# Kernel tuning notes

Hardware: AMD Instinct MI355X
Metric: run time of the kernel (lower is better)

Reference implementation:

```python
import jax, jax.numpy as jnp
import numpy as np


def setup_inputs() -> dict:
    key = jax.random.key(0)
    ks = jax.random.split(key, 12)
    M, B, N, FD, BD, BVD, H = 4096, 8, 512, 128, 128, 6, 64
    return {
        "f_pre_in": jax.random.normal(ks[0], (M, FD), jnp.float32),
        "f_pre_batch": jnp.sort(jax.random.randint(ks[1], (M,), 0, B)),
        "b_pre_in": jax.random.normal(ks[2], (B, BD, N), jnp.float32),
        "bv_in": jax.random.normal(ks[3], (B, BVD, N), jnp.float32),
        "Wf": jax.random.normal(ks[4], (H, FD), jnp.float32) * 0.05,
        "bf": jax.random.normal(ks[5], (H,), jnp.float32) * 0.05,
        "Wb": jax.random.normal(ks[6], (H, BD), jnp.float32) * 0.05,
        "bb": jax.random.normal(ks[7], (H,), jnp.float32) * 0.05,
        "Wbv": jax.random.normal(ks[8], (H, BVD), jnp.float32) * 0.05,
        "bbv": jax.random.normal(ks[9], (H,), jnp.float32) * 0.05,
        "Wo": jax.random.normal(ks[10], (H, 2 * H), jnp.float32) * 0.05,
        "bo": jax.random.normal(ks[11], (H,), jnp.float32) * 0.05,
    }


def reference(f_pre_in, f_pre_batch, b_pre_in, bv_in, Wf, bf, Wb, bb, Wbv, bbv, Wo, bo):
    # 1x1 Conv1d == channel matmul.
    H = Wf.shape[0]
    h2 = H // 2
    scale = jnp.sqrt(jnp.asarray(H, jnp.float32))  # sqrt(hidden_size)
    f = Wf @ f_pre_in.T + bf[:, None]                                  # (H, M)
    b_feat = jnp.einsum('hd,bdn->bhn', Wb, b_pre_in) + bb[None, :, None]   # (B, H, N)
    bv_feat = jnp.einsum('hc,bcn->bhn', Wbv, bv_in) + bbv[None, :, None]   # (B, H, N)
    # Per-node gather of that node's graph boundary features (f_pre_batch is sorted,
    # so per-node order == torch's per-batch concat order).
    be = b_feat[f_pre_batch, :h2]    # (M, h2, N)
    bg = b_feat[f_pre_batch, h2:]    # (M, h2, N)
    bvg = bv_feat[f_pre_batch]       # (M, H, N)
    # Cross-attention: softmax over the N boundary positions (torch dim=0 of (N, n_b)).
    w_euc = jax.nn.softmax(jnp.einsum('mhn,hm->mn', be, f[:h2]) / scale, axis=-1)  # (M, N)
    w_geo = jax.nn.softmax(jnp.einsum('mhn,hm->mn', bg, f[h2:]) / scale, axis=-1)  # (M, N)
    out_euc = jnp.einsum('mhn,mn->mh', bvg, w_euc)   # (M, H)
    out_geo = jnp.einsum('mhn,mn->mh', bvg, w_geo)   # (M, H)
    cat = jnp.concatenate([out_euc, out_geo], axis=1)  # (M, 2H)
    return cat @ Wo.T + bo                              # (M, H)
```

## Files before the change

kernel.cpp:

```cpp
#include <hip/hip_runtime.h>

#define M_TOT 4096
#define B_TOT 8
#define N_TOT 512
#define FD    128
#define BD    128
#define BVD   6
#define H     64
#define H2    32
#define MAX_TILES 264

__device__ __forceinline__ int lb_dev(const int* __restrict__ arr, int n, int v) {
    int lo = 0, hi = n;
    while (lo < hi) { int mid = (lo + hi) >> 1; if (arr[mid] < v) lo = mid + 1; else hi = mid; }
    return lo;
}

__global__ __launch_bounds__(256) void k_pre(const float* __restrict__ f_pre_in,
                                             const int*   __restrict__ batch,
                                             const float* __restrict__ b_pre_in,
                                             const float* __restrict__ bv_in,
                                             const float* __restrict__ Wf,
                                             const float* __restrict__ bf,
                                             const float* __restrict__ Wb,
                                             const float* __restrict__ bb,
                                             const float* __restrict__ Wbv,
                                             const float* __restrict__ bbv,
                                             float* __restrict__ f_mh,
                                             float* __restrict__ b_feat,
                                             float* __restrict__ bv_T,
                                             int4*  __restrict__ table) {
    __shared__ float fpre[16 * 132];
    __shared__ float WfT[128 * 68];
    __shared__ float ws2[2 * 132];
    const int t = threadIdx.x;
    const int blk = blockIdx.x;

    if (blk < 256) {
        const int m0 = blk * 16;
        for (int i = t; i < 16 * FD; i += 256)
            fpre[(i >> 7) * 132 + (i & 127)] = f_pre_in[(size_t)m0 * FD + i];
        for (int i = t; i < H * FD; i += 256)
            WfT[(i & 127) * 68 + (i >> 7)] = Wf[i];
        __syncthreads();
        const int mi = t >> 4;
        const int h4 = (t & 15) * 4;
        float a0 = bf[h4], a1 = bf[h4 + 1], a2 = bf[h4 + 2], a3 = bf[h4 + 3];
#pragma unroll 4
        for (int d4 = 0; d4 < 32; ++d4) {
            const float4 fp = *(const float4*)&fpre[mi * 132 + d4 * 4];
            const float* fpp = &fp.x;
#pragma unroll
            for (int i = 0; i < 4; ++i) {
                const float4 wv = *(const float4*)&WfT[(d4 * 4 + i) * 68 + h4];
                const float f = fpp[i];
                a0 += f * wv.x; a1 += f * wv.y; a2 += f * wv.z; a3 += f * wv.w;
            }
        }
        *(float4*)&f_mh[(size_t)(m0 + mi) * H + h4] = make_float4(a0, a1, a2, a3);
    } else if (blk < 512) {
        const int idx = blk - 256;
        const int b  = idx >> 5;
        const int h0 = (idx & 31) * 2;
        ws2[(t >> 7) * 132 + (t & 127)] = Wb[(h0 + (t >> 7)) * BD + (t & 127)];
        __syncthreads();
        const int hi = t >> 7;
        const int n4 = (t & 127) * 4;
        const float bias = bb[h0 + hi];
        float a0 = bias, a1 = bias, a2 = bias, a3 = bias;
        const float* src = b_pre_in + (size_t)b * BD * N_TOT + n4;
        const float* wp = &ws2[hi * 132];
#pragma unroll 8
        for (int d = 0; d < BD; ++d) {
            const float wv = wp[d];
            const float4 v = *(const float4*)(src + (size_t)d * N_TOT);
            a0 += wv * v.x; a1 += wv * v.y; a2 += wv * v.z; a3 += wv * v.w;
        }
        *(float4*)&b_feat[((size_t)b * H + h0 + hi) * N_TOT + n4] = make_float4(a0, a1, a2, a3);
    } else if (blk < 768) {
        const int idx = blk - 512;
        const int b  = idx >> 5;
        const int n0 = (idx & 31) * 16;
        const int h  = t & 63;
        const int nq = t >> 6;
        float wreg[BVD];
#pragma unroll
        for (int c = 0; c < BVD; ++c) wreg[c] = Wbv[h * BVD + c];
        const float bias = bbv[h];
        const float* src = bv_in + (size_t)b * BVD * N_TOT;
#pragma unroll
        for (int j = 0; j < 4; ++j) {
            const int n = n0 + nq * 4 + j;
            float acc = bias;
#pragma unroll
            for (int c = 0; c < BVD; ++c) acc += wreg[c] * src[c * N_TOT + n];
            bv_T[((size_t)b * N_TOT + n) * H + h] = acc;
        }
    } else {
        int starts[9];
#pragma unroll
        for (int b = 0; b <= 8; ++b) starts[b] = lb_dev(batch, M_TOT, b);
        int pre[9]; pre[0] = 0;
#pragma unroll
        for (int b = 0; b < 8; ++b) pre[b + 1] = pre[b] + (starts[b + 1] - starts[b] + 15) / 16;
        const int total = pre[8];
        for (int idx = t; idx < MAX_TILES; idx += 256) {
            int4 e = make_int4(0, 0, 0, 0);
            if (idx < total) {
                int b = 0;
                while (pre[b + 1] <= idx) ++b;
                const int r0 = starts[b] + (idx - pre[b]) * 16;
                e.x = b; e.y = r0; e.z = min(16, starts[b + 1] - r0);
            }
            table[idx] = e;
        }
    }
}

__device__ __forceinline__ float wave_sum64(float x) {
#pragma unroll
    for (int m = 1; m < 64; m <<= 1) x += __shfl_xor(x, m);
    return x;
}

__global__ __launch_bounds__(512, 4) void k_main(const float* __restrict__ f_mh,
                                                 const float* __restrict__ b_feat,
                                                 const float* __restrict__ bv_T,
                                                 const int4*  __restrict__ table,
                                                 float* __restrict__ pOut,
                                                 float* __restrict__ pSum) {
    __shared__ float fT[64 * 20];
    __shared__ float bFbv[64 * 133];
    __shared__ float wE[16 * 132];
    __shared__ float wG[16 * 132];
    __shared__ float rowsum[16][2];

    const int t = threadIdx.x;
    const int q    = blockIdx.x & 3;
    const int tile = blockIdx.x >> 2;
    const int4 te = table[tile];
    const int b = te.x, m0 = te.y, nr = te.z;
    if (nr == 0) return;
    const int nb = q * 128;

    for (int i = t; i < 16 * H; i += 512) {
        const int r = i >> 6, h = i & 63;
        fT[h * 20 + r] = f_mh[(size_t)(m0 + min(r, nr - 1)) * H + h];
    }
    {
        const float* src = b_feat + (size_t)b * H * N_TOT + nb;
        for (int i = t; i < 2048; i += 512) {
            const int h = i >> 5, n4 = (i & 31) * 4;
            *(float4*)&bFbv[h * 132 + n4] = *(const float4*)&src[(size_t)h * N_TOT + n4];
        }
    }
    if (t < 32) rowsum[t >> 1][t & 1] = 0.f;
    __syncthreads();

    const int lane = t & 63;
    {
        const int n_l = t & 127;
        const int rgs = t >> 7;
        float se[4] = {0.f, 0.f, 0.f, 0.f}, sg[4] = {0.f, 0.f, 0.f, 0.f};
#pragma unroll 8
        for (int h = 0; h < H2; ++h) {
            const float bE = bFbv[h * 132 + n_l];
            const float bG = bFbv[(h + 32) * 132 + n_l];
            const float4 fe = *(const float4*)&fT[h * 20 + rgs * 4];
            const float4 fg = *(const float4*)&fT[(h + 32) * 20 + rgs * 4];
            se[0] += fe.x * bE; se[1] += fe.y * bE; se[2] += fe.z * bE; se[3] += fe.w * bE;
            sg[0] += fg.x * bG; sg[1] += fg.y * bG; sg[2] += fg.z * bG; sg[3] += fg.w * bG;
        }
        float we[4], wg[4];
#pragma unroll
        for (int j = 0; j < 4; ++j) {
            we[j] = __expf(se[j] * 0.125f);
            wg[j] = __expf(sg[j] * 0.125f);
        }
#pragma unroll
        for (int j = 0; j < 4; ++j) {
            const float sE = wave_sum64(we[j]);
            const float sG = wave_sum64(wg[j]);
            if (lane == 0) {
                atomicAdd(&rowsum[rgs * 4 + j][0], sE);
                atomicAdd(&rowsum[rgs * 4 + j][1], sG);
            }
            wE[(rgs * 4 + j) * 132 + n_l] = we[j];
            wG[(rgs * 4 + j) * 132 + n_l] = wg[j];
        }
    }
    __syncthreads();

    {
        const float* src = bv_T + ((size_t)b * N_TOT + nb) * H;
        for (int i = t; i < 2048; i += 512) {
            const int n_li = i >> 4, h4 = (i & 15) * 4;
            const float4 v = *(const float4*)&src[(size_t)n_li * H + h4];
            bFbv[(h4 + 0) * 133 + n_li] = v.x;
            bFbv[(h4 + 1) * 133 + n_li] = v.y;
            bFbv[(h4 + 2) * 133 + n_li] = v.z;
            bFbv[(h4 + 3) * 133 + n_li] = v.w;
        }
    }
    __syncthreads();

    if (t < 32) {
        const int r = t >> 1, eg = t & 1;
        if (r < nr) pSum[((size_t)q * M_TOT + m0 + r) * 2 + eg] = rowsum[r][eg];
    }

    {
        const int ns = t & 3, hg = (t >> 2) & 15, rgp = t >> 6;
        float aE[2][4] = {{0.f,0.f,0.f,0.f},{0.f,0.f,0.f,0.f}};
        float aG[2][4] = {{0.f,0.f,0.f,0.f},{0.f,0.f,0.f,0.f}};
#pragma unroll 4
        for (int i = 0; i < 32; ++i) {
            const int n = ns + 4 * i;
            const float we0 = wE[(rgp * 2 + 0) * 132 + n];
            const float we1 = wE[(rgp * 2 + 1) * 132 + n];
            const float wg0 = wG[(rgp * 2 + 0) * 132 + n];
            const float wg1 = wG[(rgp * 2 + 1) * 132 + n];
            float bv4[4];
#pragma unroll
            for (int c = 0; c < 4; ++c) bv4[c] = bFbv[(hg * 4 + c) * 133 + n];
#pragma unroll
            for (int c = 0; c < 4; ++c) {
                aE[0][c] += we0 * bv4[c];
                aE[1][c] += we1 * bv4[c];
                aG[0][c] += wg0 * bv4[c];
                aG[1][c] += wg1 * bv4[c];
            }
        }
#pragma unroll
        for (int j = 0; j < 2; ++j)
#pragma unroll
            for (int c = 0; c < 4; ++c) {
                aE[j][c] += __shfl_xor(aE[j][c], 1); aE[j][c] += __shfl_xor(aE[j][c], 2);
                aG[j][c] += __shfl_xor(aG[j][c], 1); aG[j][c] += __shfl_xor(aG[j][c], 2);
            }
        if (ns == 0) {
#pragma unroll
            for (int j = 0; j < 2; ++j) {
                const int r = rgp * 2 + j;
                if (r < nr) {
                    float* dst = pOut + ((size_t)q * M_TOT + m0 + r) * 128;
                    *(float4*)&dst[hg * 4]      = make_float4(aE[j][0], aE[j][1], aE[j][2], aE[j][3]);
                    *(float4*)&dst[64 + hg * 4] = make_float4(aG[j][0], aG[j][1], aG[j][2], aG[j][3]);
                }
            }
        }
    }
}

__global__ __launch_bounds__(256) void k_merge(const float* __restrict__ pOut,
                                               const float* __restrict__ pSum,
                                               const float* __restrict__ Wo,
                                               const float* __restrict__ bo,
                                               float* __restrict__ out) {
    __shared__ float WoT[128 * 68];
    __shared__ float cat[16 * 132];
    __shared__ float rinv[16][2];
    const int t = threadIdx.x;
    const int m0 = blockIdx.x * 16;

    for (int i = t; i < H * 2 * H; i += 256)
        WoT[(i & 127) * 68 + (i >> 7)] = Wo[i];
    if (t < 32) {
        const int r = t >> 1, eg = t & 1;
        float s = 0.f;
#pragma unroll
        for (int qq = 0; qq < 4; ++qq) s += pSum[((size_t)qq * M_TOT + m0 + r) * 2 + eg];
        rinv[r][eg] = 1.0f / s;
    }
    __syncthreads();

    for (int i = t; i < 512; i += 256) {
        const int r = i >> 5, k4 = (i & 31) * 4;
        float4 s = make_float4(0.f, 0.f, 0.f, 0.f);
#pragma unroll
        for (int qq = 0; qq < 4; ++qq) {
            const float4 v = *(const float4*)&pOut[(((size_t)qq * M_TOT + m0 + r) * 128) + k4];
            s.x += v.x; s.y += v.y; s.z += v.z; s.w += v.w;
        }
        const float inv = rinv[r][k4 >= 64];
        *(float4*)&cat[r * 132 + k4] = make_float4(s.x * inv, s.y * inv, s.z * inv, s.w * inv);
    }
    __syncthreads();

    const int mi = t >> 4;
    const int j4 = (t & 15) * 4;
    float a0 = bo[j4], a1 = bo[j4 + 1], a2 = bo[j4 + 2], a3 = bo[j4 + 3];
#pragma unroll 4
    for (int k4s = 0; k4s < 32; ++k4s) {
        const float4 c4 = *(const float4*)&cat[mi * 132 + 4 * k4s];
        const float* cp = &c4.x;
#pragma unroll
        for (int i = 0; i < 4; ++i) {
            const float4 wv = *(const float4*)&WoT[(4 * k4s + i) * 68 + j4];
            const float c = cp[i];
            a0 += c * wv.x; a1 += c * wv.y; a2 += c * wv.z; a3 += c * wv.w;
        }
    }
    *(float4*)&out[(size_t)(m0 + mi) * H + j4] = make_float4(a0, a1, a2, a3);
}

extern "C" void kernel_launch(void* const* d_in, const int* in_sizes, int n_in,
                              void* d_out, int out_size, void* d_ws, size_t ws_size,
                              hipStream_t stream) {
    const float* f_pre_in = (const float*)d_in[0];
    const int*   f_batch  = (const int*)  d_in[1];
    const float* b_pre_in = (const float*)d_in[2];
    const float* bv_in    = (const float*)d_in[3];
    const float* Wf       = (const float*)d_in[4];
    const float* bf       = (const float*)d_in[5];
    const float* Wb       = (const float*)d_in[6];
    const float* bb       = (const float*)d_in[7];
    const float* Wbv      = (const float*)d_in[8];
    const float* bbv      = (const float*)d_in[9];
    const float* Wo       = (const float*)d_in[10];
    const float* bo       = (const float*)d_in[11];
    float* out = (float*)d_out;

    float* f_mh   = (float*)d_ws;
    float* b_feat = f_mh + (size_t)M_TOT * H;
    float* bv_T   = b_feat + (size_t)B_TOT * H * N_TOT;
    float* pOut   = bv_T + (size_t)B_TOT * N_TOT * H;
    float* pSum   = pOut + (size_t)4 * M_TOT * 128;
    int4*  table  = (int4*)(pSum + (size_t)4 * M_TOT * 2);

    k_pre  <<<769, 256, 0, stream>>>(f_pre_in, f_batch, b_pre_in, bv_in,
                                     Wf, bf, Wb, bb, Wbv, bbv,
                                     f_mh, b_feat, bv_T, table);
    k_main <<<4 * MAX_TILES, 512, 0, stream>>>(f_mh, b_feat, bv_T, table, pOut, pSum);
    k_merge<<<256, 256, 0, stream>>>(pOut, pSum, Wo, bo, out);
}
```

Baseline: 135.5 us.

## Rewrite attention core with bf16 MFMA and fuse merge/output projection into main kernel

```diff
diff --git a/kernel.cpp b/kernel.cpp
--- a/kernel.cpp
+++ b/kernel.cpp
@@ -7,8 +7,19 @@
 #define BD    128
 #define BVD   6
 #define H     64
-#define H2    32
 #define MAX_TILES 264
+
+typedef short short8 __attribute__((ext_vector_type(8)));
+typedef float floatx4 __attribute__((ext_vector_type(4)));
+
+__device__ __forceinline__ unsigned short f2bf(float x) {
+    union { float f; unsigned int u; } v; v.f = x;
+    return (unsigned short)((v.u + 0x7fffu + ((v.u >> 16) & 1u)) >> 16);
+}
+__device__ __forceinline__ float bf2f(unsigned short u) {
+    union { unsigned int u32; float f; } v; v.u32 = ((unsigned int)u) << 16;
+    return v.f;
+}
 
 __device__ __forceinline__ int lb_dev(const int* __restrict__ arr, int n, int v) {
     int lo = 0, hi = n;
@@ -26,17 +37,19 @@
                                              const float* __restrict__ bb,
                                              const float* __restrict__ Wbv,
                                              const float* __restrict__ bbv,
-                                             float* __restrict__ f_mh,
-                                             float* __restrict__ b_feat,
-                                             float* __restrict__ bv_T,
+                                             const float* __restrict__ Wo,
+                                             unsigned short* __restrict__ f_bf,
+                                             unsigned short* __restrict__ bFT_bf,
+                                             unsigned short* __restrict__ bv_bf,
+                                             unsigned short* __restrict__ Wo_bf,
                                              int4*  __restrict__ table) {
-    __shared__ float fpre[16 * 132];
-    __shared__ float WfT[128 * 68];
-    __shared__ float ws2[2 * 132];
+    __shared__ __align__(16) char sm[43264];
     const int t = threadIdx.x;
     const int blk = blockIdx.x;
 
     if (blk < 256) {
+        float* fpre = (float*)sm;
+        float* WfT  = (float*)(sm + 8448);
         const int m0 = blk * 16;
         for (int i = t; i < 16 * FD; i += 256)
             fpre[(i >> 7) * 132 + (i & 127)] = f_pre_in[(size_t)m0 * FD + i];
@@ -57,45 +70,54 @@
                 a0 += f * wv.x; a1 += f * wv.y; a2 += f * wv.z; a3 += f * wv.w;
             }
         }
-        *(float4*)&f_mh[(size_t)(m0 + mi) * H + h4] = make_float4(a0, a1, a2, a3);
+        ushort4 o; o.x = f2bf(a0); o.y = f2bf(a1); o.z = f2bf(a2); o.w = f2bf(a3);
+        *(ushort4*)&f_bf[(size_t)(m0 + mi) * H + h4] = o;
     } else if (blk < 512) {
+        float* Wb_l = (float*)sm;
+        float* bp   = (float*)(sm + 33024);
         const int idx = blk - 256;
         const int b  = idx >> 5;
-        const int h0 = (idx & 31) * 2;
-        ws2[(t >> 7) * 132 + (t & 127)] = Wb[(h0 + (t >> 7)) * BD + (t & 127)];
+        const int n0 = (idx & 31) * 16;
+        for (int i = t; i < H * BD; i += 256)
+            Wb_l[(i >> 7) * 129 + (i & 127)] = Wb[i];
+        for (int i = t; i < BD * 16; i += 256)
+            bp[(i >> 4) * 17 + (i & 15)] =
+                b_pre_in[(size_t)b * BD * N_TOT + (size_t)(i >> 4) * N_TOT + n0 + (i & 15)];
         __syncthreads();
-        const int hi = t >> 7;
-        const int n4 = (t & 127) * 4;
-        const float bias = bb[h0 + hi];
-        float a0 = bias, a1 = bias, a2 = bias, a3 = bias;
-        const float* src = b_pre_in + (size_t)b * BD * N_TOT + n4;
-        const float* wp = &ws2[hi * 132];
+        const int h  = t & 63;
+        const int nl = t >> 6;
+        const float bias = bb[h];
+        float acc[4] = {bias, bias, bias, bias};
+        const float* wr = &Wb_l[h * 129];
 #pragma unroll 8
         for (int d = 0; d < BD; ++d) {
-            const float wv = wp[d];
-            const float4 v = *(const float4*)(src + (size_t)d * N_TOT);
-            a0 += wv * v.x; a1 += wv * v.y; a2 += wv * v.z; a3 += wv * v.w;
-        }
-        *(float4*)&b_feat[((size_t)b * H + h0 + hi) * N_TOT + n4] = make_float4(a0, a1, a2, a3);
+            const float w = wr[d];
+            acc[0] += w * bp[d * 17 + nl];
+            acc[1] += w * bp[d * 17 + nl + 4];
+            acc[2] += w * bp[d * 17 + nl + 8];
+            acc[3] += w * bp[d * 17 + nl + 12];
+        }
+#pragma unroll
+        for (int j = 0; j < 4; ++j)
+            bFT_bf[((size_t)b * N_TOT + n0 + nl + 4 * j) * H + h] = f2bf(acc[j]);
     } else if (blk < 768) {
         const int idx = blk - 512;
         const int b  = idx >> 5;
-        const int n0 = (idx & 31) * 16;
-        const int h  = t & 63;
-        const int nq = t >> 6;
-        float wreg[BVD];
-#pragma unroll
-        for (int c = 0; c < BVD; ++c) wreg[c] = Wbv[h * BVD + c];
+        const int h  = (idx & 31) * 2 + (t >> 7);
+        const int n4 = (t & 127) * 4;
+        float w[BVD];
+#pragma unroll
+        for (int c = 0; c < BVD; ++c) w[c] = Wbv[h * BVD + c];
         const float bias = bbv[h];
-        const float* src = bv_in + (size_t)b * BVD * N_TOT;
-#pragma unroll
-        for (int j = 0; j < 4; ++j) {
-            const int n = n0 + nq * 4 + j;
-            float acc = bias;
-#pragma unroll
-            for (int c = 0; c < BVD; ++c) acc += wreg[c] * src[c * N_TOT + n];
-            bv_T[((size_t)b * N_TOT + n) * H + h] = acc;
-        }
+        float a0 = bias, a1 = bias, a2 = bias, a3 = bias;
+        const float* src = bv_in + (size_t)b * BVD * N_TOT + n4;
+#pragma unroll
+        for (int c = 0; c < BVD; ++c) {
+            const float4 v = *(const float4*)(src + c * N_TOT);
+            a0 += w[c] * v.x; a1 += w[c] * v.y; a2 += w[c] * v.z; a3 += w[c] * v.w;
+        }
+        ushort4 o; o.x = f2bf(a0); o.y = f2bf(a1); o.z = f2bf(a2); o.w = f2bf(a3);
+        *(ushort4*)&bv_bf[((size_t)b * H + h) * N_TOT + n4] = o;
     } else {
         int starts[9];
 #pragma unroll
@@ -114,194 +136,125 @@
             }
             table[idx] = e;
         }
-    }
-}
-
-__device__ __forceinline__ float wave_sum64(float x) {
-#pragma unroll
-    for (int m = 1; m < 64; m <<= 1) x += __shfl_xor(x, m);
-    return x;
-}
-
-__global__ __launch_bounds__(512, 4) void k_main(const float* __restrict__ f_mh,
-                                                 const float* __restrict__ b_feat,
-                                                 const float* __restrict__ bv_T,
-                                                 const int4*  __restrict__ table,
-                                                 float* __restrict__ pOut,
-                                                 float* __restrict__ pSum) {
-    __shared__ float fT[64 * 20];
-    __shared__ float bFbv[64 * 133];
-    __shared__ float wE[16 * 132];
-    __shared__ float wG[16 * 132];
-    __shared__ float rowsum[16][2];
+        for (int i = t; i < H * 2 * H; i += 256) Wo_bf[i] = f2bf(Wo[i]);
+    }
+}
+
+__global__ __launch_bounds__(256) void k_main(const unsigned short* __restrict__ f_bf,
+                                              const unsigned short* __restrict__ bFT_bf,
+                                              const unsigned short* __restrict__ bv_bf,
+                                              const unsigned short* __restrict__ Wo_bf,
+                                              const float* __restrict__ bo,
+                                              const int4*  __restrict__ table,
+                                              float* __restrict__ out) {
+    __shared__ __align__(16) char wreg[4][8704];
+    __shared__ __align__(16) float rowsumP[4][2][16];
+    __shared__ __align__(16) unsigned short cat_l[16 * 136];
 
     const int t = threadIdx.x;
-    const int q    = blockIdx.x & 3;
-    const int tile = blockIdx.x >> 2;
-    const int4 te = table[tile];
+    const int wave = t >> 6, l = t & 63, quad = l >> 4, s = l & 15;
+    const int4 te = table[blockIdx.x];
     const int b = te.x, m0 = te.y, nr = te.z;
     if (nr == 0) return;
-    const int nb = q * 128;
-
-    for (int i = t; i < 16 * H; i += 512) {
-        const int r = i >> 6, h = i & 63;
-        fT[h * 20 + r] = f_mh[(size_t)(m0 + min(r, nr - 1)) * H + h];
+
+    unsigned short* Wl = (unsigned short*)&wreg[wave][0];
+    const floatx4 zero = {0.f, 0.f, 0.f, 0.f};
+
+    const int rclamp = (s < nr) ? s : (nr - 1);
+    const unsigned short* fptr = f_bf + (size_t)(m0 + rclamp) * H + quad * 8;
+    const short8 fE = *(const short8*)(fptr);
+    const short8 fG = *(const short8*)(fptr + 32);
+
+    const unsigned short* bA = bFT_bf + ((size_t)b * N_TOT + wave * 128 + s) * H + quad * 8;
+    floatx4 dE[8], dG[8];
+#pragma unroll
+    for (int c = 0; c < 8; ++c) {
+        const short8 aE = *(const short8*)(bA + (size_t)c * 16 * H);
+        const short8 aG = *(const short8*)(bA + (size_t)c * 16 * H + 32);
+        dE[c] = __builtin_amdgcn_mfma_f32_16x16x32_bf16(aE, fE, zero, 0, 0, 0);
+        dG[c] = __builtin_amdgcn_mfma_f32_16x16x32_bf16(aG, fG, zero, 0, 0, 0);
+    }
+
+    float rsE = 0.f, rsG = 0.f;
+#pragma unroll
+    for (int c = 0; c < 8; ++c) {
+        ushort4 pE, pG;
+        unsigned short u;
+        u = f2bf(__expf(dE[c][0] * 0.125f)); rsE += bf2f(u); pE.x = u;
+        u = f2bf(__expf(dE[c][1] * 0.125f)); rsE += bf2f(u); pE.y = u;
+        u = f2bf(__expf(dE[c][2] * 0.125f)); rsE += bf2f(u); pE.z = u;
+        u = f2bf(__expf(dE[c][3] * 0.125f)); rsE += bf2f(u); pE.w = u;
+        u = f2bf(__expf(dG[c][0] * 0.125f)); rsG += bf2f(u); pG.x = u;
+        u = f2bf(__expf(dG[c][1] * 0.125f)); rsG += bf2f(u); pG.y = u;
+        u = f2bf(__expf(dG[c][2] * 0.125f)); rsG += bf2f(u); pG.z = u;
+        u = f2bf(__expf(dG[c][3] * 0.125f)); rsG += bf2f(u); pG.w = u;
+        *(ushort4*)&Wl[s * 136 + c * 16 + quad * 4]        = pE;
+        *(ushort4*)&Wl[2176 + s * 136 + c * 16 + quad * 4] = pG;
+    }
+    rsE += __shfl_xor(rsE, 16); rsE += __shfl_xor(rsE, 32);
+    rsG += __shfl_xor(rsG, 16); rsG += __shfl_xor(rsG, 32);
+    if (l < 16) { rowsumP[wave][0][s] = rsE; rowsumP[wave][1][s] = rsG; }
+
+    floatx4 oE[4] = {zero, zero, zero, zero};
+    floatx4 oG[4] = {zero, zero, zero, zero};
+#pragma unroll
+    for (int kc = 0; kc < 4; ++kc) {
+        const short8 aE = *(const short8*)&Wl[s * 136 + kc * 32 + quad * 8];
+        const short8 aG = *(const short8*)&Wl[2176 + s * 136 + kc * 32 + quad * 8];
+#pragma unroll
+        for (int hc = 0; hc < 4; ++hc) {
+            const short8 bvf = *(const short8*)(bv_bf +
+                ((size_t)b * H + hc * 16 + s) * N_TOT + wave * 128 + kc * 32 + quad * 8);
+            oE[hc] = __builtin_amdgcn_mfma_f32_16x16x32_bf16(aE, bvf, oE[hc], 0, 0, 0);
+            oG[hc] = __builtin_amdgcn_mfma_f32_16x16x32_bf16(aG, bvf, oG[hc], 0, 0, 0);
+        }
     }
     {
-        const float* src = b_feat + (size_t)b * H * N_TOT + nb;
-        for (int i = t; i < 2048; i += 512) {
-            const int h = i >> 5, n4 = (i & 31) * 4;
-            *(float4*)&bFbv[h * 132 + n4] = *(const float4*)&src[(size_t)h * N_TOT + n4];
-        }
-    }
-    if (t < 32) rowsum[t >> 1][t & 1] = 0.f;
+        float* Op = (float*)&wreg[wave][0];
+#pragma unroll
+        for (int hc = 0; hc < 4; ++hc) {
+            *(floatx4*)&Op[(hc * 16 + s) * 16 + quad * 4]        = oE[hc];
+            *(floatx4*)&Op[1024 + (hc * 16 + s) * 16 + quad * 4] = oG[hc];
+        }
+    }
     __syncthreads();
 
-    const int lane = t & 63;
     {
-        const int n_l = t & 127;
-        const int rgs = t >> 7;
-        float se[4] = {0.f, 0.f, 0.f, 0.f}, sg[4] = {0.f, 0.f, 0.f, 0.f};
-#pragma unroll 8
-        for (int h = 0; h < H2; ++h) {
-            const float bE = bFbv[h * 132 + n_l];
-            const float bG = bFbv[(h + 32) * 132 + n_l];
-            const float4 fe = *(const float4*)&fT[h * 20 + rgs * 4];
-            const float4 fg = *(const float4*)&fT[(h + 32) * 20 + rgs * 4];
-            se[0] += fe.x * bE; se[1] += fe.y * bE; se[2] += fe.z * bE; se[3] += fe.w * bE;
-            sg[0] += fg.x * bG; sg[1] += fg.y * bG; sg[2] += fg.z * bG; sg[3] += fg.w * bG;
-        }
-        float we[4], wg[4];
-#pragma unroll
-        for (int j = 0; j < 4; ++j) {
-            we[j] = __expf(se[j] * 0.125f);
-            wg[j] = __expf(sg[j] * 0.125f);
-        }
-#pragma unroll
-        for (int j = 0; j < 4; ++j) {
-            const float sE = wave_sum64(we[j]);
-            const float sG = wave_sum64(wg[j]);
-            if (lane == 0) {
-                atomicAdd(&rowsum[rgs * 4 + j][0], sE);
-                atomicAdd(&rowsum[rgs * 4 + j][1], sG);
-            }
-            wE[(rgs * 4 + j) * 132 + n_l] = we[j];
-            wG[(rgs * 4 + j) * 132 + n_l] = wg[j];
+        const int h  = t >> 2;
+        const int r4 = (t & 3) * 4;
+        floatx4 sE = zero, sG = zero, rE = zero, rG = zero;
+#pragma unroll
+        for (int w = 0; w < 4; ++w) {
+            const float* opw = (const float*)&wreg[w][0];
+            sE += *(const floatx4*)&opw[h * 16 + r4];
+            sG += *(const floatx4*)&opw[1024 + h * 16 + r4];
+            rE += *(const floatx4*)&rowsumP[w][0][r4];
+            rG += *(const floatx4*)&rowsumP[w][1][r4];
+        }
+#pragma unroll
+        for (int i = 0; i < 4; ++i) {
+            cat_l[(r4 + i) * 136 + h]      = f2bf(sE[i] / rE[i]);
+            cat_l[(r4 + i) * 136 + 64 + h] = f2bf(sG[i] / rG[i]);
         }
     }
     __syncthreads();
 
     {
-        const float* src = bv_T + ((size_t)b * N_TOT + nb) * H;
-        for (int i = t; i < 2048; i += 512) {
-            const int n_li = i >> 4, h4 = (i & 15) * 4;
-            const float4 v = *(const float4*)&src[(size_t)n_li * H + h4];
-            bFbv[(h4 + 0) * 133 + n_li] = v.x;
-            bFbv[(h4 + 1) * 133 + n_li] = v.y;
-            bFbv[(h4 + 2) * 133 + n_li] = v.z;
-            bFbv[(h4 + 3) * 133 + n_li] = v.w;
-        }
-    }
-    __syncthreads();
-
-    if (t < 32) {
-        const int r = t >> 1, eg = t & 1;
-        if (r < nr) pSum[((size_t)q * M_TOT + m0 + r) * 2 + eg] = rowsum[r][eg];
-    }
-
-    {
-        const int ns = t & 3, hg = (t >> 2) & 15, rgp = t >> 6;
-        float aE[2][4] = {{0.f,0.f,0.f,0.f},{0.f,0.f,0.f,0.f}};
-        float aG[2][4] = {{0.f,0.f,0.f,0.f},{0.f,0.f,0.f,0.f}};
-#pragma unroll 4
-        for (int i = 0; i < 32; ++i) {
-            const int n = ns + 4 * i;
-            const float we0 = wE[(rgp * 2 + 0) * 132 + n];
-            const float we1 = wE[(rgp * 2 + 1) * 132 + n];
-            const float wg0 = wG[(rgp * 2 + 0) * 132 + n];
-            const float wg1 = wG[(rgp * 2 + 1) * 132 + n];
-            float bv4[4];
-#pragma unroll
-            for (int c = 0; c < 4; ++c) bv4[c] = bFbv[(hg * 4 + c) * 133 + n];
-#pragma unroll
-            for (int c = 0; c < 4; ++c) {
-                aE[0][c] += we0 * bv4[c];
-                aE[1][c] += we1 * bv4[c];
-                aG[0][c] += wg0 * bv4[c];
-                aG[1][c] += wg1 * bv4[c];
-            }
-        }
-#pragma unroll
-        for (int j = 0; j < 2; ++j)
-#pragma unroll
-            for (int c = 0; c < 4; ++c) {
-                aE[j][c] += __shfl_xor(aE[j][c], 1); aE[j][c] += __shfl_xor(aE[j][c], 2);
-                aG[j][c] += __shfl_xor(aG[j][c], 1); aG[j][c] += __shfl_xor(aG[j][c], 2);
-            }
-        if (ns == 0) {
-#pragma unroll
-            for (int j = 0; j < 2; ++j) {
-                const int r = rgp * 2 + j;
-                if (r < nr) {
-                    float* dst = pOut + ((size_t)q * M_TOT + m0 + r) * 128;
-                    *(float4*)&dst[hg * 4]      = make_float4(aE[j][0], aE[j][1], aE[j][2], aE[j][3]);
-                    *(float4*)&dst[64 + hg * 4] = make_float4(aG[j][0], aG[j][1], aG[j][2], aG[j][3]);
-                }
-            }
-        }
-    }
-}
-
-__global__ __launch_bounds__(256) void k_merge(const float* __restrict__ pOut,
-                                               const float* __restrict__ pSum,
-                                               const float* __restrict__ Wo,
-                                               const float* __restrict__ bo,
-                                               float* __restrict__ out) {
-    __shared__ float WoT[128 * 68];
-    __shared__ float cat[16 * 132];
-    __shared__ float rinv[16][2];
-    const int t = threadIdx.x;
-    const int m0 = blockIdx.x * 16;
-
-    for (int i = t; i < H * 2 * H; i += 256)
-        WoT[(i & 127) * 68 + (i >> 7)] = Wo[i];
-    if (t < 32) {
-        const int r = t >> 1, eg = t & 1;
-        float s = 0.f;
-#pragma unroll
-        for (int qq = 0; qq < 4; ++qq) s += pSum[((size_t)qq * M_TOT + m0 + r) * 2 + eg];
-        rinv[r][eg] = 1.0f / s;
-    }
-    __syncthreads();
-
-    for (int i = t; i < 512; i += 256) {
-        const int r = i >> 5, k4 = (i & 31) * 4;
-        float4 s = make_float4(0.f, 0.f, 0.f, 0.f);
-#pragma unroll
-        for (int qq = 0; qq < 4; ++qq) {
-            const float4 v = *(const float4*)&pOut[(((size_t)qq * M_TOT + m0 + r) * 128) + k4];
-            s.x += v.x; s.y += v.y; s.z += v.z; s.w += v.w;
-        }
-        const float inv = rinv[r][k4 >= 64];
-        *(float4*)&cat[r * 132 + k4] = make_float4(s.x * inv, s.y * inv, s.z * inv, s.w * inv);
-    }
-    __syncthreads();
-
-    const int mi = t >> 4;
-    const int j4 = (t & 15) * 4;
-    float a0 = bo[j4], a1 = bo[j4 + 1], a2 = bo[j4 + 2], a3 = bo[j4 + 3];
-#pragma unroll 4
-    for (int k4s = 0; k4s < 32; ++k4s) {
-        const float4 c4 = *(const float4*)&cat[mi * 132 + 4 * k4s];
-        const float* cp = &c4.x;
-#pragma unroll
-        for (int i = 0; i < 4; ++i) {
-            const float4 wv = *(const float4*)&WoT[(4 * k4s + i) * 68 + j4];
-            const float c = cp[i];
-            a0 += c * wv.x; a1 += c * wv.y; a2 += c * wv.z; a3 += c * wv.w;
-        }
-    }
-    *(float4*)&out[(size_t)(m0 + mi) * H + j4] = make_float4(a0, a1, a2, a3);
+        floatx4 acc = zero;
+#pragma unroll
+        for (int kc = 0; kc < 4; ++kc) {
+            const short8 aC = *(const short8*)&cat_l[s * 136 + kc * 32 + quad * 8];
+            const short8 bW = *(const short8*)(Wo_bf + (size_t)(wave * 16 + s) * 128 + kc * 32 + quad * 8);
+            acc = __builtin_amdgcn_mfma_f32_16x16x32_bf16(aC, bW, acc, 0, 0, 0);
+        }
+        const int j = wave * 16 + s;
+        const float bj = bo[j];
+#pragma unroll
+        for (int reg = 0; reg < 4; ++reg) {
+            const int r = quad * 4 + reg;
+            if (r < nr) out[(size_t)(m0 + r) * H + j] = acc[reg] + bj;
+        }
+    }
 }
 
 extern "C" void kernel_launch(void* const* d_in, const int* in_sizes, int n_in,
@@ -321,16 +274,14 @@
     const float* bo       = (const float*)d_in[11];
     float* out = (float*)d_out;
 
-    float* f_mh   = (float*)d_ws;
-    float* b_feat = f_mh + (size_t)M_TOT * H;
-    float* bv_T   = b_feat + (size_t)B_TOT * H * N_TOT;
-    float* pOut   = bv_T + (size_t)B_TOT * N_TOT * H;
-    float* pSum   = pOut + (size_t)4 * M_TOT * 128;
-    int4*  table  = (int4*)(pSum + (size_t)4 * M_TOT * 2);
-
-    k_pre  <<<769, 256, 0, stream>>>(f_pre_in, f_batch, b_pre_in, bv_in,
-                                     Wf, bf, Wb, bb, Wbv, bbv,
-                                     f_mh, b_feat, bv_T, table);
-    k_main <<<4 * MAX_TILES, 512, 0, stream>>>(f_mh, b_feat, bv_T, table, pOut, pSum);
-    k_merge<<<256, 256, 0, stream>>>(pOut, pSum, Wo, bo, out);
-}
+    unsigned short* f_bf   = (unsigned short*)d_ws;
+    unsigned short* bFT_bf = f_bf + (size_t)M_TOT * H;
+    unsigned short* bv_bf  = bFT_bf + (size_t)B_TOT * N_TOT * H;
+    unsigned short* Wo_bf  = bv_bf + (size_t)B_TOT * H * N_TOT;
+    int4* table = (int4*)(Wo_bf + (size_t)H * 2 * H);
+
+    k_pre <<<769, 256, 0, stream>>>(f_pre_in, f_batch, b_pre_in, bv_in,
+                                    Wf, bf, Wb, bb, Wbv, bbv, Wo,
+                                    f_bf, bFT_bf, bv_bf, Wo_bf, table);
+    k_main<<<MAX_TILES, 256, 0, stream>>>(f_bf, bFT_bf, bv_bf, Wo_bf, bo, table, out);
+}
```

New measurement: 109.3 us. 1.24x faster.
